# Kernel tuning notes

Hardware: AMD Instinct MI355X
Metric: run time of the kernel (lower is better)

The kernel has to match this reference:

```python
import jax, jax.numpy as jnp
import numpy as np

B, S, D, H = 2, 2048, 1024, 16
DH = D // H

def setup_inputs() -> dict:
    key = jax.random.key(0)
    k1, k2, k3, k4 = jax.random.split(key, 4)
    x = jax.random.normal(k1, (B, S, D), dtype=jnp.float32)
    # flax Dense kernels: [in_features, out_features]
    w_qkv = jax.random.normal(k2, (D, 3 * D), dtype=jnp.float32) / np.sqrt(D)
    w_out = jax.random.normal(k3, (D, D), dtype=jnp.float32) / np.sqrt(D)
    b_out = jax.random.normal(k4, (D,), dtype=jnp.float32) * 0.01
    return {"x": x, "w_qkv": w_qkv, "w_out": w_out, "b_out": b_out}

def reference(x, w_qkv, w_out, b_out):
    b, s, d = x.shape
    h, dh = H, d // H
    qkv = jnp.einsum('bsd,de->bse', x, w_qkv)           # [B,S,3D]
    qkv = qkv.reshape(b, s, 3, h, dh)
    qkv = jnp.transpose(qkv, (2, 0, 3, 1, 4))            # [3,B,H,S,DH]
    q, k, v = qkv[0], qkv[1], qkv[2]
    attn = jnp.einsum('bhqd,bhkd->bhqk', q, k) / jnp.sqrt(jnp.float32(dh))
    attn = jax.nn.softmax(attn, axis=-1)                 # [B,H,S,S]
    y = jnp.einsum('bhqk,bhkd->bhqd', attn, v)           # [B,H,S,DH]
    y = jnp.transpose(y, (0, 2, 1, 3)).reshape(b, s, d)  # [B,S,D]
    return jnp.einsum('bsd,de->bse', y, w_out) + b_out
```

## Files before the change

kernel.cpp:

```cpp
#include <hip/hip_runtime.h>
#include <stdint.h>

typedef __bf16 bf16_t;
typedef __bf16 bf16x8 __attribute__((ext_vector_type(8)));
typedef float f32x4 __attribute__((ext_vector_type(4)));
typedef float f32x16 __attribute__((ext_vector_type(16)));
typedef unsigned short u16;
typedef unsigned short u16x8 __attribute__((ext_vector_type(8)));
typedef unsigned int u32;
typedef unsigned int u32x4 __attribute__((ext_vector_type(4)));

#define DEVI __device__ __forceinline__


DEVI u16 bits(float f) { bf16_t h = (bf16_t)f; return __builtin_bit_cast(u16, h); }

DEVI void gld16(const void* g, void* l) {
  __builtin_amdgcn_global_load_lds(
      (const __attribute__((address_space(1))) unsigned int*)g,
      (__attribute__((address_space(3))) unsigned int*)l, 16, 0, 0);
}

DEVI bf16x8 ldsr(const u16* s, int row, int cg) {
  const int byte = row * 128 + ((cg ^ (row & 7)) << 4);
  return *(const bf16x8*)((const char*)s + byte);
}

DEVI bf16x8 ldsrV(const u16* s, int row, int cg) {
  const int byte = row * 256 + ((cg ^ (row & 15)) << 4);
  return *(const bf16x8*)((const char*)s + byte);
}

DEVI float exp2v(float x) { return __builtin_amdgcn_exp2f(x); }

DEVI u32 cvtpk(float lo, float hi) {
  u32 r;
  asm("v_cvt_pk_bf16_f32 %0, %1, %2" : "=v"(r) : "v"(lo), "v"(hi));
  return r;
}

#define MFMA16(a, b, c) __builtin_amdgcn_mfma_f32_16x16x32_bf16(a, b, c, 0, 0, 0)
#define MFMA32(a, b, c) __builtin_amdgcn_mfma_f32_32x32x16_bf16(a, b, c, 0, 0, 0)

#define MKFRAG(dst, S, B)                                              \
  {                                                                    \
    u32 a_ = cvtpk(S[(B) + 0], S[(B) + 1]);                            \
    u32 b_ = cvtpk(S[(B) + 4], S[(B) + 5]);                            \
    u32 c_ = cvtpk(S[(B) + 2], S[(B) + 3]);                            \
    u32 d_ = cvtpk(S[(B) + 6], S[(B) + 7]);                            \
    asm("v_permlane32_swap_b32 %0, %1" : "+v"(a_), "+v"(b_));          \
    asm("v_permlane32_swap_b32 %0, %1" : "+v"(c_), "+v"(d_));          \
    u32x4 u_ = {a_, c_, b_, d_};                                       \
    dst = __builtin_bit_cast(bf16x8, u_);                              \
  }

__global__ void __launch_bounds__(256) cvt8(const float* __restrict__ in,
                                            u16* __restrict__ out, int n8) {
  const int i = blockIdx.x * 256 + threadIdx.x;
  if (i >= n8) return;
  const f32x4* p = (const f32x4*)in;
  const f32x4 a = p[2 * i], b = p[2 * i + 1];
  u16x8 o;
#pragma unroll
  for (int j = 0; j < 4; ++j) { o[j] = bits(a[j]); o[4 + j] = bits(b[j]); }
  *(u16x8*)(out + (size_t)i * 8) = o;
}

__global__ void __launch_bounds__(256) tconv(const float* __restrict__ in,
                                             u16* __restrict__ out, int K, int N) {
  __shared__ float T[64][65];
  const int k0 = blockIdx.x * 64, n0 = blockIdx.y * 64;
  const int tid = threadIdx.x;
#pragma unroll
  for (int i = 0; i < 4; ++i) {
    const int c = i * 256 + tid;
    const int row = c >> 4, c4 = c & 15;
    const f32x4 v = *(const f32x4*)(in + (size_t)(k0 + row) * N + n0 + c4 * 4);
#pragma unroll
    for (int j = 0; j < 4; ++j) T[row][c4 * 4 + j] = v[j];
  }
  __syncthreads();
#pragma unroll
  for (int i = 0; i < 2; ++i) {
    const int c = i * 256 + tid;
    const int nrow = c >> 3, k8 = c & 7;
    u16x8 o;
#pragma unroll
    for (int j = 0; j < 8; ++j) o[j] = bits(T[k8 * 8 + j][nrow]);
    *(u16x8*)(out + (size_t)(n0 + nrow) * K + k0 + k8 * 8) = o;
  }
}

__global__ void __launch_bounds__(256) vtrans(const u16* __restrict__ Vrm,
                                              u16* __restrict__ Vt) {
  __shared__ u16 T[64][72];
  const int s0 = blockIdx.x * 64;
  const int bh = blockIdx.y;
  const int tid = threadIdx.x;
#pragma unroll
  for (int i = 0; i < 2; ++i) {
    const int c = i * 256 + tid, srow = c >> 3, c8 = c & 7;
    const u16x8 v = *(const u16x8*)(Vrm + ((size_t)bh * 2048 + s0 + srow) * 64 + c8 * 8);
#pragma unroll
    for (int j = 0; j < 8; ++j) T[srow][c8 * 8 + j] = v[j];
  }
  __syncthreads();
#pragma unroll
  for (int i = 0; i < 2; ++i) {
    const int c = i * 256 + tid, dr = c >> 3, s8 = c & 7;
    u16x8 o;
#pragma unroll
    for (int j = 0; j < 8; ++j) o[j] = T[s8 * 8 + j][dr];
    *(u16x8*)(Vt + ((size_t)bh * 64 + dr) * 2048 + s0 + s8 * 8) = o;
  }
}

template <int BN>
DEVI void gemm_core(const u16* __restrict__ A, const u16* __restrict__ Bt,
                    u16* As, u16* Bs, int m0, int n0, int Kdim,
                    f32x4 (&acc)[4][BN / 32]) {
  const int NF = BN / 32;
  const int tid = threadIdx.x;
  const int l = tid & 63, w = tid >> 6;
  const int lr = l & 15, lh = l >> 4;
  const int wr = w >> 1, wc = w & 1;
  for (int kt = 0; kt < Kdim; kt += 64) {
#pragma unroll
    for (int i = 0; i < 4; ++i) {
      const int cb = i * 256 + w * 64;
      const int c = cb + l;
      const int row = c >> 3;
      const int col = ((c & 7) ^ (row & 7)) << 3;
      gld16(A + (size_t)(m0 + row) * Kdim + kt + col, As + (size_t)cb * 8);
    }
#pragma unroll
    for (int i = 0; i < BN / 32; ++i) {
      const int cb = i * 256 + w * 64;
      const int c = cb + l;
      const int row = c >> 3;
      const int col = ((c & 7) ^ (row & 7)) << 3;
      gld16(Bt + (size_t)(n0 + row) * Kdim + kt + col, Bs + (size_t)cb * 8);
    }
    __syncthreads();
#pragma unroll
    for (int kk = 0; kk < 2; ++kk) {
      bf16x8 af[4], bfr[NF];
#pragma unroll
      for (int m = 0; m < 4; ++m) af[m] = ldsr(As, wr * 64 + m * 16 + lr, kk * 4 + lh);
#pragma unroll
      for (int n = 0; n < NF; ++n)
        bfr[n] = ldsr(Bs, wc * (BN / 2) + n * 16 + lr, kk * 4 + lh);
#pragma unroll
      for (int m = 0; m < 4; ++m)
#pragma unroll
        for (int n = 0; n < NF; ++n)
          acc[m][n] = MFMA16(af[m], bfr[n], acc[m][n]);
    }
    __syncthreads();
  }
}


DEVI void stage_half(const u16* __restrict__ G, int row0, int kt, u16* dst) {
  const int tid = threadIdx.x;
  const int l = tid & 63, wv = tid >> 6;
  const u16* gp = G + (size_t)row0 * 1024 + kt;
#pragma unroll
  for (int i = 0; i < 2; ++i) {
    const int cb = i * 512 + wv * 64;
    const int c = cb + l;
    const int rih = c >> 3;
    const int col = ((c & 7) ^ (rih & 7)) << 3;
    gld16(gp + (size_t)rih * 1024 + col, dst + cb * 8);
  }
}

template <bool SA1, bool SB2, int VM>
DEVI void qkv_tile(const u16* __restrict__ A, const u16* __restrict__ Bt,
                   int m0, int n0, int ktA1, int ktB2,
                   u16* Ac, u16* Bc, u16* An, f32x4 (&acc)[8][4]) {
  const int tid = threadIdx.x;
  const int l = tid & 63, wv = tid >> 6;
  const int lr = l & 15, lh = l >> 4;
  const int wr = wv >> 2, wc = wv & 3;
  const int ab = wr * 128, bb = wc * 64;
  bf16x8 a0[8], a1[8], b0[4], b1[4];
#pragma unroll
  for (int m = 0; m < 4; ++m)
#pragma unroll
    for (int kk = 0; kk < 2; ++kk)
      a0[m * 2 + kk] = ldsr(Ac, ab + m * 16 + lr, kk * 4 + lh);
#pragma unroll
  for (int n = 0; n < 2; ++n)
#pragma unroll
    for (int kk = 0; kk < 2; ++kk)
      b0[n * 2 + kk] = ldsr(Bc, bb + n * 16 + lr, kk * 4 + lh);
  if (SA1) stage_half(A, m0, ktA1, An);
  __builtin_amdgcn_s_barrier();
  asm volatile("s_waitcnt lgkmcnt(0)" ::: "memory");
  __builtin_amdgcn_sched_barrier(0);
  __builtin_amdgcn_s_setprio(1);
#pragma unroll
  for (int m = 0; m < 4; ++m)
#pragma unroll
    for (int n = 0; n < 2; ++n)
#pragma unroll
      for (int kk = 0; kk < 2; ++kk)
        acc[m][n] = MFMA16(a0[m * 2 + kk], b0[n * 2 + kk], acc[m][n]);
  __builtin_amdgcn_s_setprio(0);
  __builtin_amdgcn_s_barrier();
#pragma unroll
  for (int n = 0; n < 2; ++n)
#pragma unroll
    for (int kk = 0; kk < 2; ++kk)
      b1[n * 2 + kk] = ldsr(Bc, bb + 32 + n * 16 + lr, kk * 4 + lh);
  if (SA1) stage_half(A, m0 + 128, ktA1, An + 8192);
  __builtin_amdgcn_s_barrier();
  asm volatile("s_waitcnt lgkmcnt(0)" ::: "memory");
  __builtin_amdgcn_sched_barrier(0);
  __builtin_amdgcn_s_setprio(1);
#pragma unroll
  for (int m = 0; m < 4; ++m)
#pragma unroll
    for (int n = 0; n < 2; ++n)
#pragma unroll
      for (int kk = 0; kk < 2; ++kk)
        acc[m][2 + n] = MFMA16(a0[m * 2 + kk], b1[n * 2 + kk], acc[m][2 + n]);
  __builtin_amdgcn_s_setprio(0);
  __builtin_amdgcn_s_barrier();
#pragma unroll
  for (int m = 0; m < 4; ++m)
#pragma unroll
    for (int kk = 0; kk < 2; ++kk)
      a1[m * 2 + kk] = ldsr(Ac, ab + 64 + m * 16 + lr, kk * 4 + lh);
  if (SB2) stage_half(Bt, n0, ktB2, Bc);
  __builtin_amdgcn_s_barrier();
  asm volatile("s_waitcnt lgkmcnt(0)" ::: "memory");
  __builtin_amdgcn_sched_barrier(0);
  __builtin_amdgcn_s_setprio(1);
#pragma unroll
  for (int m = 0; m < 4; ++m)
#pragma unroll
    for (int n = 0; n < 2; ++n)
#pragma unroll
      for (int kk = 0; kk < 2; ++kk)
        acc[4 + m][n] = MFMA16(a1[m * 2 + kk], b0[n * 2 + kk], acc[4 + m][n]);
  __builtin_amdgcn_s_setprio(0);
  __builtin_amdgcn_s_barrier();
  if (SB2) stage_half(Bt, n0 + 128, ktB2, Bc + 8192);
  __builtin_amdgcn_s_barrier();
  __builtin_amdgcn_s_setprio(1);
#pragma unroll
  for (int m = 0; m < 4; ++m)
#pragma unroll
    for (int n = 0; n < 2; ++n)
#pragma unroll
      for (int kk = 0; kk < 2; ++kk)
        acc[4 + m][2 + n] = MFMA16(a1[m * 2 + kk], b1[n * 2 + kk], acc[4 + m][2 + n]);
  __builtin_amdgcn_s_setprio(0);
  if (VM == 4) asm volatile("s_waitcnt vmcnt(4)" ::: "memory");
  else if (VM == 0) asm volatile("s_waitcnt vmcnt(0)" ::: "memory");
  __builtin_amdgcn_s_barrier();
}

__global__ void __launch_bounds__(512, 2) gemm_qkv_k(const u16* __restrict__ A,
                                                     const u16* __restrict__ Bt,
                                                     u16* __restrict__ Qb,
                                                     u16* __restrict__ Kb,
                                                     u16* __restrict__ Vb) {
  __shared__ u16 LA[2][16384], LB[2][16384];
  const int bid = blockIdx.x;
  const int g = bid & 7, w24 = bid >> 3;
  const int mt = (g >> 1) * 4 + (w24 & 3);
  const int nt = (g & 1) * 6 + (w24 >> 2);
  const int m0 = mt * 256, n0 = nt * 256;

  stage_half(A, m0, 0, LA[0]);
  stage_half(A, m0 + 128, 0, LA[0] + 8192);
  stage_half(Bt, n0, 0, LB[0]);
  stage_half(Bt, n0 + 128, 0, LB[0] + 8192);
  stage_half(Bt, n0, 64, LB[1]);
  stage_half(Bt, n0 + 128, 64, LB[1] + 8192);
  asm volatile("s_waitcnt vmcnt(4)" ::: "memory");
  __builtin_amdgcn_s_barrier();

  f32x4 acc[8][4] = {};
  u16 *Ac = LA[0], *Bc = LB[0], *An = LA[1], *Bn = LB[1];
#pragma unroll 1
  for (int t = 0; t < 14; ++t) {
    qkv_tile<true, true, 4>(A, Bt, m0, n0, (t + 1) * 64, (t + 2) * 64, Ac, Bc, An, acc);
    u16* tp = Ac; Ac = An; An = tp;
    tp = Bc; Bc = Bn; Bn = tp;
  }
  qkv_tile<true, false, 0>(A, Bt, m0, n0, 15 * 64, 0, Ac, Bc, An, acc);
  { u16* tp = Ac; Ac = An; An = tp; tp = Bc; Bc = Bn; Bn = tp; }
  qkv_tile<false, false, -1>(A, Bt, m0, n0, 0, 0, Ac, Bc, An, acc);

  const int tid = threadIdx.x;
  const int l = tid & 63, wv = tid >> 6;
  const int lr = l & 15, lh = l >> 4;
  const int wr = wv >> 2, wc = wv & 3;
#pragma unroll
  for (int n = 0; n < 4; ++n) {
    const int ng = n0 + wc * 64 + n * 16 + lr;
    const int sel = ng >> 10, h = (ng >> 6) & 15, dh = ng & 63;
    u16* dst = sel == 0 ? Qb : (sel == 1 ? Kb : Vb);
    const float qs = (sel == 0) ? 0.125f * 1.44269504f : 1.0f;
#pragma unroll
    for (int m = 0; m < 8; ++m) {
#pragma unroll
      for (int r = 0; r < 4; ++r) {
        const int mg = m0 + wr * 128 + m * 16 + lh * 4 + r;
        const int b = mg >> 11, s = mg & 2047;
        dst[((size_t)(b * 16 + h) * 2048 + s) * 64 + dh] = bits(acc[m][n][r] * qs);
      }
    }
  }
}

__global__ void __launch_bounds__(256) gemm_out_k(const u16* __restrict__ A,
                                                  const u16* __restrict__ Bt,
                                                  const float* __restrict__ bias,
                                                  float* __restrict__ out) {
  __shared__ u16 As[128 * 64], Bs[64 * 64];
  const int m0 = blockIdx.y * 128, n0 = blockIdx.x * 64;
  f32x4 acc[4][2] = {};
  gemm_core<64>(A, Bt, As, Bs, m0, n0, 1024, acc);
  const int tid = threadIdx.x;
  const int l = tid & 63, w = tid >> 6;
  const int lr = l & 15, lh = l >> 4;
  const int wr = w >> 1, wc = w & 1;
#pragma unroll
  for (int n = 0; n < 2; ++n) {
    const int ng = n0 + wc * 32 + n * 16 + lr;
    const float bv = bias[ng];
#pragma unroll
    for (int m = 0; m < 4; ++m) {
#pragma unroll
      for (int r = 0; r < 4; ++r) {
        const int mg = m0 + wr * 64 + m * 16 + lh * 4 + r;
        out[(size_t)mg * 1024 + ng] = acc[m][n][r] + bv;
      }
    }
  }
}

__global__ void __launch_bounds__(512, 4) attn_k(const u16* __restrict__ Qb,
                                                 const u16* __restrict__ Kb,
                                                 const u16* __restrict__ Vt,
                                                 u16* __restrict__ Yb) {
  __shared__ char smem[65536];
  u16* const KsA = (u16*)smem;
  u16* const KsB = (u16*)(smem + 16384);
  u16* const VsA = (u16*)(smem + 32768);
  u16* const VsB = (u16*)(smem + 49152);

  const int tid = threadIdx.x;
  const int l = tid & 63, w = tid >> 6;
  const int lq = l & 31, hi = l >> 5;
  const int qw = w & 3;
  const int khalf = w >> 2;
  const int i0 = blockIdx.x;
  const int bid = (i0 & 7) * 64 + (i0 >> 3);
  const int bh = bid >> 4, qt = bid & 15;

  const u16* Qp = Qb + ((size_t)bh * 2048 + qt * 128 + qw * 32 + lq) * 64;
  bf16x8 qf0 = *(const bf16x8*)(Qp + hi * 8);
  bf16x8 qf1 = *(const bf16x8*)(Qp + 16 + hi * 8);
  bf16x8 qf2 = *(const bf16x8*)(Qp + 32 + hi * 8);
  bf16x8 qf3 = *(const bf16x8*)(Qp + 48 + hi * 8);

  const u16* Kbase = Kb + (size_t)bh * 2048 * 64;
  const u16* Vbase = Vt + (size_t)bh * 64 * 2048;

  bf16x8 ones;
#pragma unroll
  for (int j = 0; j < 8; ++j) ones[j] = (bf16_t)1.0f;

  f32x16 acc0 = {}, acc1 = {};
  f32x16 accs = {};

#define STAGE(Ksb, Vsb, kv0)                                               \
  {                                                                        \
    _Pragma("unroll") for (int ii = 0; ii < 2; ++ii) {                     \
      const int cb = ii * 512 + w * 64;                                    \
      const int c = cb + l;                                                \
      const int krow = c >> 3;                                             \
      const int kcol = ((c & 7) ^ (krow & 7)) << 3;                        \
      gld16(Kbase + (size_t)((kv0) + krow) * 64 + kcol, (Ksb) + cb * 8);   \
      const int vrow = c >> 4;                                             \
      const int vcol = ((c & 15) ^ (vrow & 15)) << 3;                      \
      gld16(Vbase + (size_t)vrow * 2048 + (kv0) + vcol, (Vsb) + cb * 8);   \
    }                                                                      \
  }

  STAGE(KsA, VsA, 0);
  asm volatile("s_waitcnt vmcnt(0)" ::: "memory");
  __builtin_amdgcn_s_barrier();

  bf16x8 pc0 = ones, pc1 = ones;
  int cur = 0;
#pragma unroll 1
  for (int t = 0; t < 16; ++t) {
    const u16* Ksc = cur ? KsB : KsA;
    const u16* Vsc = cur ? VsB : VsA;
    const u16* Vsp = cur ? VsA : VsB;

    if (t > 0) {
      __builtin_amdgcn_s_setprio(1);
      accs = MFMA32(pc0, ones, accs);
      acc0 = MFMA32(pc0, ldsrV(Vsp, lq, khalf * 8 + 4 + hi), acc0);
      acc1 = MFMA32(pc0, ldsrV(Vsp, 32 + lq, khalf * 8 + 4 + hi), acc1);
      accs = MFMA32(pc1, ones, accs);
      acc0 = MFMA32(pc1, ldsrV(Vsp, lq, khalf * 8 + 6 + hi), acc0);
      acc1 = MFMA32(pc1, ldsrV(Vsp, 32 + lq, khalf * 8 + 6 + hi), acc1);
      __builtin_amdgcn_s_setprio(0);
      asm volatile("s_waitcnt vmcnt(0)" ::: "memory");
      __builtin_amdgcn_s_barrier();
    }
    if (t + 1 < 16) STAGE((cur ? KsA : KsB), (cur ? VsA : VsB), (t + 1) * 128);

    f32x16 s0 = {}, s1 = {};
    __builtin_amdgcn_s_setprio(1);
    s0 = MFMA32(ldsr(Ksc, khalf * 64 + lq, hi), qf0, s0);
    s0 = MFMA32(ldsr(Ksc, khalf * 64 + lq, 2 + hi), qf1, s0);
    s0 = MFMA32(ldsr(Ksc, khalf * 64 + lq, 4 + hi), qf2, s0);
    s0 = MFMA32(ldsr(Ksc, khalf * 64 + lq, 6 + hi), qf3, s0);
    s1 = MFMA32(ldsr(Ksc, khalf * 64 + 32 + lq, hi), qf0, s1);
    s0[0] = exp2v(s0[0]); s0[1] = exp2v(s0[1]); s0[2] = exp2v(s0[2]); s0[3] = exp2v(s0[3]);
    s1 = MFMA32(ldsr(Ksc, khalf * 64 + 32 + lq, 2 + hi), qf1, s1);
    s0[4] = exp2v(s0[4]); s0[5] = exp2v(s0[5]); s0[6] = exp2v(s0[6]); s0[7] = exp2v(s0[7]);
    s1 = MFMA32(ldsr(Ksc, khalf * 64 + 32 + lq, 4 + hi), qf2, s1);
    s0[8] = exp2v(s0[8]); s0[9] = exp2v(s0[9]); s0[10] = exp2v(s0[10]); s0[11] = exp2v(s0[11]);
    s1 = MFMA32(ldsr(Ksc, khalf * 64 + 32 + lq, 6 + hi), qf3, s1);
    s0[12] = exp2v(s0[12]); s0[13] = exp2v(s0[13]); s0[14] = exp2v(s0[14]); s0[15] = exp2v(s0[15]);
    __builtin_amdgcn_s_setprio(0);

    bf16x8 pa0, pa1;
    MKFRAG(pa0, s0, 0);
    MKFRAG(pa1, s0, 8);

    __builtin_amdgcn_s_setprio(1);
    accs = MFMA32(pa0, ones, accs);
    s1[0] = exp2v(s1[0]); s1[1] = exp2v(s1[1]); s1[2] = exp2v(s1[2]);
    acc0 = MFMA32(pa0, ldsrV(Vsc, lq, khalf * 8 + hi), acc0);
    s1[3] = exp2v(s1[3]); s1[4] = exp2v(s1[4]); s1[5] = exp2v(s1[5]);
    acc1 = MFMA32(pa0, ldsrV(Vsc, 32 + lq, khalf * 8 + hi), acc1);
    s1[6] = exp2v(s1[6]); s1[7] = exp2v(s1[7]); s1[8] = exp2v(s1[8]);
    accs = MFMA32(pa1, ones, accs);
    s1[9] = exp2v(s1[9]); s1[10] = exp2v(s1[10]); s1[11] = exp2v(s1[11]);
    acc0 = MFMA32(pa1, ldsrV(Vsc, lq, khalf * 8 + 2 + hi), acc0);
    s1[12] = exp2v(s1[12]); s1[13] = exp2v(s1[13]); s1[14] = exp2v(s1[14]);
    acc1 = MFMA32(pa1, ldsrV(Vsc, 32 + lq, khalf * 8 + 2 + hi), acc1);
    s1[15] = exp2v(s1[15]);
    __builtin_amdgcn_s_setprio(0);

    MKFRAG(pc0, s1, 0);
    MKFRAG(pc1, s1, 8);
    cur ^= 1;
  }
  {
    const u16* Vsp = cur ? VsA : VsB;
    accs = MFMA32(pc0, ones, accs);
    acc0 = MFMA32(pc0, ldsrV(Vsp, lq, khalf * 8 + 4 + hi), acc0);
    acc1 = MFMA32(pc0, ldsrV(Vsp, 32 + lq, khalf * 8 + 4 + hi), acc1);
    accs = MFMA32(pc1, ones, accs);
    acc0 = MFMA32(pc1, ldsrV(Vsp, lq, khalf * 8 + 6 + hi), acc0);
    acc1 = MFMA32(pc1, ldsrV(Vsp, 32 + lq, khalf * 8 + 6 + hi), acc1);
  }
#undef STAGE
  __syncthreads();

  float* const F = (float*)smem;
  float* const Fp = F + (size_t)(tid & 255) * 49;
  if (khalf) {
#pragma unroll
    for (int r = 0; r < 16; ++r) {
      Fp[r] = acc0[r];
      Fp[16 + r] = acc1[r];
      Fp[32 + r] = accs[r];
    }
  }
  __syncthreads();
  if (khalf) return;
#pragma unroll
  for (int r = 0; r < 16; ++r) {
    acc0[r] += Fp[r];
    acc1[r] += Fp[16 + r];
    accs[r] += Fp[32 + r];
  }

  const int b = bh >> 4, h = bh & 15;
#pragma unroll
  for (int r = 0; r < 16; ++r) {
    const float sd = 1.0f / accs[r];
    const int row = (r & 3) + 8 * (r >> 2) + 4 * hi;
    const int sq = qt * 128 + qw * 32 + row;
    u16* yp = Yb + ((size_t)b * 2048 + sq) * 1024 + h * 64;
    yp[lq] = bits(acc0[r] * sd);
    yp[32 + lq] = bits(acc1[r] * sd);
  }
}

extern "C" void kernel_launch(void* const* d_in, const int* in_sizes, int n_in,
                              void* d_out, int out_size, void* d_ws, size_t ws_size,
                              hipStream_t stream) {
  (void)in_sizes; (void)n_in; (void)out_size; (void)ws_size;
  const float* x     = (const float*)d_in[0];
  const float* w_qkv = (const float*)d_in[1];
  const float* w_out = (const float*)d_in[2];
  const float* b_out = (const float*)d_in[3];
  float* out = (float*)d_out;

  char* ws = (char*)d_ws;
  u16* xb    = (u16*)(ws);
  u16* wqkvT = (u16*)(ws + 8388608);
  u16* woutT = (u16*)(ws + 14680064);
  u16* Qb    = (u16*)(ws + 16777216);
  u16* Kb    = (u16*)(ws + 25165824);
  u16* Vrm   = (u16*)(ws + 33554432);
  u16* Vt    = (u16*)(ws + 41943040);
  u16* Yb    = xb;

  cvt8<<<2048, 256, 0, stream>>>(x, xb, 4194304 / 8);
  tconv<<<dim3(16, 48), 256, 0, stream>>>(w_qkv, wqkvT, 1024, 3072);
  tconv<<<dim3(16, 16), 256, 0, stream>>>(w_out, woutT, 1024, 1024);
  gemm_qkv_k<<<192, 512, 0, stream>>>(xb, wqkvT, Qb, Kb, Vrm);
  vtrans<<<dim3(32, 32), 256, 0, stream>>>(Vrm, Vt);
  attn_k<<<512, 512, 0, stream>>>(Qb, Kb, Vt, Yb);
  gemm_out_k<<<dim3(16, 32), 256, 0, stream>>>(Yb, woutT, b_out, out);
}
```

Baseline: 111.7 us.

## Fuse V transpose into QKV epilogue, merge weight converts, widen out-GEMM tile

The QKV GEMM epilogue now writes V directly in transposed [bh, dh, s] layout, which removes the separate vtrans kernel and its round trip through global memory. The two weight transpose-convert launches are merged into a single tconv2 kernel that selects its source by blockIdx.y. The output projection GEMM moves from 128x64 to 128x128 tiles, which halves its grid and raises per-block reuse. The cost is scattered 2-byte stores for V with a large stride, which may coalesce poorly, and lower occupancy and parallelism for the out GEMM.

```diff
diff --git a/kernel.cpp b/kernel.cpp
--- a/kernel.cpp
+++ b/kernel.cpp
@@ -66,10 +66,17 @@
   *(u16x8*)(out + (size_t)i * 8) = o;
 }
 
-__global__ void __launch_bounds__(256) tconv(const float* __restrict__ in,
-                                             u16* __restrict__ out, int K, int N) {
+__global__ void __launch_bounds__(256) tconv2(const float* __restrict__ wqkv,
+                                              const float* __restrict__ wout,
+                                              u16* __restrict__ oqkv,
+                                              u16* __restrict__ oout) {
   __shared__ float T[64][65];
-  const int k0 = blockIdx.x * 64, n0 = blockIdx.y * 64;
+  const int K = 1024;
+  const int sel = blockIdx.y >= 48;
+  const float* in = sel ? wout : wqkv;
+  u16* out = sel ? oout : oqkv;
+  const int N = sel ? 1024 : 3072;
+  const int k0 = blockIdx.x * 64, n0 = (sel ? blockIdx.y - 48 : blockIdx.y) * 64;
   const int tid = threadIdx.x;
 #pragma unroll
   for (int i = 0; i < 4; ++i) {
@@ -88,30 +95,6 @@
 #pragma unroll
     for (int j = 0; j < 8; ++j) o[j] = bits(T[k8 * 8 + j][nrow]);
     *(u16x8*)(out + (size_t)(n0 + nrow) * K + k0 + k8 * 8) = o;
-  }
-}
-
-__global__ void __launch_bounds__(256) vtrans(const u16* __restrict__ Vrm,
-                                              u16* __restrict__ Vt) {
-  __shared__ u16 T[64][72];
-  const int s0 = blockIdx.x * 64;
-  const int bh = blockIdx.y;
-  const int tid = threadIdx.x;
-#pragma unroll
-  for (int i = 0; i < 2; ++i) {
-    const int c = i * 256 + tid, srow = c >> 3, c8 = c & 7;
-    const u16x8 v = *(const u16x8*)(Vrm + ((size_t)bh * 2048 + s0 + srow) * 64 + c8 * 8);
-#pragma unroll
-    for (int j = 0; j < 8; ++j) T[srow][c8 * 8 + j] = v[j];
-  }
-  __syncthreads();
-#pragma unroll
-  for (int i = 0; i < 2; ++i) {
-    const int c = i * 256 + tid, dr = c >> 3, s8 = c & 7;
-    u16x8 o;
-#pragma unroll
-    for (int j = 0; j < 8; ++j) o[j] = T[s8 * 8 + j][dr];
-    *(u16x8*)(Vt + ((size_t)bh * 64 + dr) * 2048 + s0 + s8 * 8) = o;
   }
 }
 
@@ -267,7 +250,7 @@
                                                      const u16* __restrict__ Bt,
                                                      u16* __restrict__ Qb,
                                                      u16* __restrict__ Kb,
-                                                     u16* __restrict__ Vb) {
+                                                     u16* __restrict__ Vtb) {
   __shared__ u16 LA[2][16384], LB[2][16384];
   const int bid = blockIdx.x;
   const int g = bid & 7, w24 = bid >> 3;
@@ -304,7 +287,6 @@
   for (int n = 0; n < 4; ++n) {
     const int ng = n0 + wc * 64 + n * 16 + lr;
     const int sel = ng >> 10, h = (ng >> 6) & 15, dh = ng & 63;
-    u16* dst = sel == 0 ? Qb : (sel == 1 ? Kb : Vb);
     const float qs = (sel == 0) ? 0.125f * 1.44269504f : 1.0f;
 #pragma unroll
     for (int m = 0; m < 8; ++m) {
@@ -312,7 +294,13 @@
       for (int r = 0; r < 4; ++r) {
         const int mg = m0 + wr * 128 + m * 16 + lh * 4 + r;
         const int b = mg >> 11, s = mg & 2047;
-        dst[((size_t)(b * 16 + h) * 2048 + s) * 64 + dh] = bits(acc[m][n][r] * qs);
+        const u16 v = bits(acc[m][n][r] * qs);
+        if (sel == 2) {
+          Vtb[((size_t)(b * 16 + h) * 64 + dh) * 2048 + s] = v;
+        } else {
+          u16* dst = sel == 0 ? Qb : Kb;
+          dst[((size_t)(b * 16 + h) * 2048 + s) * 64 + dh] = v;
+        }
       }
     }
   }
@@ -322,17 +310,17 @@
                                                   const u16* __restrict__ Bt,
                                                   const float* __restrict__ bias,
                                                   float* __restrict__ out) {
-  __shared__ u16 As[128 * 64], Bs[64 * 64];
-  const int m0 = blockIdx.y * 128, n0 = blockIdx.x * 64;
-  f32x4 acc[4][2] = {};
-  gemm_core<64>(A, Bt, As, Bs, m0, n0, 1024, acc);
+  __shared__ u16 As[128 * 64], Bs[128 * 64];
+  const int m0 = blockIdx.y * 128, n0 = blockIdx.x * 128;
+  f32x4 acc[4][4] = {};
+  gemm_core<128>(A, Bt, As, Bs, m0, n0, 1024, acc);
   const int tid = threadIdx.x;
   const int l = tid & 63, w = tid >> 6;
   const int lr = l & 15, lh = l >> 4;
   const int wr = w >> 1, wc = w & 1;
 #pragma unroll
-  for (int n = 0; n < 2; ++n) {
-    const int ng = n0 + wc * 32 + n * 16 + lr;
+  for (int n = 0; n < 4; ++n) {
+    const int ng = n0 + wc * 64 + n * 16 + lr;
     const float bv = bias[ng];
 #pragma unroll
     for (int m = 0; m < 4; ++m) {
@@ -518,15 +506,12 @@
   u16* woutT = (u16*)(ws + 14680064);
   u16* Qb    = (u16*)(ws + 16777216);
   u16* Kb    = (u16*)(ws + 25165824);
-  u16* Vrm   = (u16*)(ws + 33554432);
   u16* Vt    = (u16*)(ws + 41943040);
   u16* Yb    = xb;
 
   cvt8<<<2048, 256, 0, stream>>>(x, xb, 4194304 / 8);
-  tconv<<<dim3(16, 48), 256, 0, stream>>>(w_qkv, wqkvT, 1024, 3072);
-  tconv<<<dim3(16, 16), 256, 0, stream>>>(w_out, woutT, 1024, 1024);
-  gemm_qkv_k<<<192, 512, 0, stream>>>(xb, wqkvT, Qb, Kb, Vrm);
-  vtrans<<<dim3(32, 32), 256, 0, stream>>>(Vrm, Vt);
+  tconv2<<<dim3(16, 64), 256, 0, stream>>>(w_qkv, w_out, wqkvT, woutT);
+  gemm_qkv_k<<<192, 512, 0, stream>>>(xb, wqkvT, Qb, Kb, Vt);
   attn_k<<<512, 512, 0, stream>>>(Qb, Kb, Vt, Yb);
-  gemm_out_k<<<dim3(16, 32), 256, 0, stream>>>(Yb, woutT, b_out, out);
-}
+  gemm_out_k<<<dim3(8, 32), 256, 0, stream>>>(Yb, woutT, b_out, out);
+}
```

Result: slower. 134.1 us (+20.0%).
